# Kernel tuning notes

Hardware: AMD Instinct MI355X
Metric: run time of the kernel (lower is better)

Reference implementation:

```python
import math
import jax, jax.numpy as jnp
import numpy as np

NO_ITEMS = 50000
EMB_DIM = 448
FEAT_DIM = 64
DIM = EMB_DIM + FEAT_DIM  # 512
N_BLOCKS = 2
B, S = 8, 2048
EPS = 1e-05


def setup_inputs() -> dict:
    key = jax.random.key(0)
    ks = jax.random.split(key, 16)
    inv = 1.0 / math.sqrt(DIM)
    inp = {
        "user_sequence": jax.random.randint(ks[0], (B, S), 0, NO_ITEMS),
        "user_sequence_features": jax.random.normal(ks[1], (B, S, FEAT_DIM), dtype=jnp.float32),
        "emb_table": jax.random.normal(ks[2], (NO_ITEMS, EMB_DIM), dtype=jnp.float32) * 0.02,
        # stacked per-block params [L, DIM, DIM] / [L, DIM]; torch Linear: y = x @ W.T + b
        "Wq": jax.random.normal(ks[3], (N_BLOCKS, DIM, DIM), dtype=jnp.float32) * inv,
        "bq": jax.random.normal(ks[4], (N_BLOCKS, DIM), dtype=jnp.float32) * inv,
        "Wk": jax.random.normal(ks[5], (N_BLOCKS, DIM, DIM), dtype=jnp.float32) * inv,
        "bk": jax.random.normal(ks[6], (N_BLOCKS, DIM), dtype=jnp.float32) * inv,
        "Wv": jax.random.normal(ks[7], (N_BLOCKS, DIM, DIM), dtype=jnp.float32) * inv,
        "bv": jax.random.normal(ks[8], (N_BLOCKS, DIM), dtype=jnp.float32) * inv,
        "W1": jax.random.normal(ks[9], (N_BLOCKS, DIM, DIM), dtype=jnp.float32) * inv,
        "b1": jax.random.normal(ks[10], (N_BLOCKS, DIM), dtype=jnp.float32) * inv,
        "W2": jax.random.normal(ks[11], (N_BLOCKS, DIM, DIM), dtype=jnp.float32) * inv,
        "b2": jax.random.normal(ks[12], (N_BLOCKS, DIM), dtype=jnp.float32) * inv,
    }
    return inp


def _seq_norm(h):
    # EmbeddingSequenceNorm: normalize over sequence axis (axis=1),
    # torch .std() is unbiased (ddof=1); note the double eps in the source.
    mean = h.mean(axis=1)                        # [B, D]
    std = jnp.std(h, axis=1, ddof=1) + 1e-05     # [B, D]
    return (h - mean[:, None, :]) / (std[:, None, :] + EPS)


def reference(user_sequence, user_sequence_features, emb_table,
              Wq, bq, Wk, bk, Wv, bv, W1, b1, W2, b2):
    emb = emb_table[user_sequence]                       # [B, S, EMB_DIM]
    feats = user_sequence_features[:, :, :FEAT_DIM]      # [B, S, FEAT_DIM]
    x = jnp.concatenate([emb, feats], axis=-1)           # [B, S, DIM]
    scale = 1.0 / math.sqrt(DIM)
    for l in range(N_BLOCKS):
        q = x @ Wq[l].T + bq[l]
        k = x @ Wk[l].T + bk[l]
        v = x @ Wv[l].T + bv[l]
        # NOTE: no softmax in the original — raw tril(QK^T * scale) @ V
        scores = jnp.einsum('bqd,bkd->bqk', q, k) * scale  # [B, S, S]
        scores = jnp.tril(scores)
        h = jnp.einsum('bqk,bkd->bqd', scores, v)
        h = _seq_norm(h)
        h = jnp.maximum(h @ W1[l].T + b1[l], 0.0) @ W2[l].T + b2[l]
        x = h
    return x[:, -1]  # [B, DIM]
```

## Files before the change

### kernel.cpp

```cpp
#include <hip/hip_runtime.h>
#include <hip/hip_bf16.h>

typedef __hip_bfloat16 BF;
typedef __bf16 v8bf __attribute__((ext_vector_type(8)));
typedef float v4f __attribute__((ext_vector_type(4)));

constexpr int SEQ = 2048;
constexpr int DIMC = 512;
constexpr int BSZ = 8;

#define GF_RELU 1
#define GF_CAUSAL 2
#define GF_KCAP 4
#define GF_QKV 8
#define GF_BATCH8 16
#define GF_HSTAT 32

#define WAIT_VM4 0x0F74
#define WAIT_VM0 0x0F70

__device__ __forceinline__ void async16(BF* lds, const BF* g) {
  __builtin_amdgcn_global_load_lds(
      (const __attribute__((address_space(1))) void*)g,
      (__attribute__((address_space(3))) void*)lds,
      16, 0, 0);
}

__global__ __launch_bounds__(256, 4) void gemm_bt(
    const BF* __restrict__ A, const BF* __restrict__ W, const float* __restrict__ bias,
    BF* __restrict__ outB, float* __restrict__ outF, BF* __restrict__ outV,
    float* __restrict__ hsum, float* __restrict__ hsq,
    int M, int N, int K, int nbx,
    long long strideA, long long strideW, long long strideC,
    float scale, int flags)
{
  const int id = blockIdx.x;
  int z, bx, by;
  if (flags & GF_BATCH8) {
    z = id & 7;
    const int t = id >> 3;
    bx = t % nbx;
    by = t / nbx;
    if (flags & GF_KCAP) by = (M >> 7) - 1 - by;
  } else {
    z = 0;
    by = (id & 7) + ((id >> 3) & 15) * 8;
    bx = id >> 7;
  }
  const int m0 = by * 128;
  const int n0 = bx * 128;
  if ((flags & GF_CAUSAL) && n0 > m0) return;

  const BF* __restrict__ Ab = A + (size_t)z * strideA;
  const BF* __restrict__ Wb = W + (size_t)z * strideW;
  const size_t coff = (size_t)z * strideC;

  const int tid = threadIdx.x;
  const int w = tid >> 6;
  const int lane = tid & 63;
  const int lane15 = lane & 15;
  const int quad = lane >> 4;
  const int wr = w >> 1, wc = w & 1;
  const int rl = lane >> 2;
  const int clsw = ((lane & 3) ^ ((rl >> 1) & 3)) << 3;

  __shared__ __align__(16) BF smem[16384];
  BF* sA = smem;
  BF* sW = smem + 8192;

  v4f acc[4][4];
  {
    v4f zero = {0.f, 0.f, 0.f, 0.f};
#pragma unroll
    for (int a = 0; a < 4; ++a)
#pragma unroll
      for (int b = 0; b < 4; ++b) acc[a][b] = zero;
  }

  int Klim = K;
  if (flags & GF_KCAP) { int kc = m0 + 128; if (kc < Klim) Klim = kc; }
  const int ksteps = Klim >> 5;

  auto stage = [&](int kk, int buf) {
    const int k0 = kk << 5;
#pragma unroll
    for (int i = 0; i < 2; ++i) {
      const int r0 = w * 32 + i * 16;
      async16(&sA[buf * 4096 + r0 * 32], Ab + (size_t)(m0 + r0 + rl) * K + (k0 + clsw));
      async16(&sW[buf * 4096 + r0 * 32], Wb + (size_t)(n0 + r0 + rl) * K + (k0 + clsw));
    }
  };

  stage(0, 0);
  const int sw = quad ^ ((lane15 >> 1) & 3);

  for (int kk = 0; kk < ksteps; ++kk) {
    const int cur = kk & 1;
    if (kk + 1 < ksteps) {
      stage(kk + 1, cur ^ 1);
      __builtin_amdgcn_s_waitcnt(WAIT_VM4);
    } else {
      __builtin_amdgcn_s_waitcnt(WAIT_VM0);
    }
    __builtin_amdgcn_s_barrier();

    v8bf aF[4], wF[4];
    const v8bf* sAv = (const v8bf*)(sA + cur * 4096);
    const v8bf* sWv = (const v8bf*)(sW + cur * 4096);
#pragma unroll
    for (int t = 0; t < 4; ++t) {
      aF[t] = sAv[(wr * 64 + t * 16 + lane15) * 4 + sw];
      wF[t] = sWv[(wc * 64 + t * 16 + lane15) * 4 + sw];
    }
#pragma unroll
    for (int mt = 0; mt < 4; ++mt)
#pragma unroll
      for (int nt = 0; nt < 4; ++nt)
        acc[mt][nt] = __builtin_amdgcn_mfma_f32_16x16x32_bf16(aF[mt], wF[nt], acc[mt][nt], 0, 0, 0);
    __builtin_amdgcn_s_barrier();
  }

  if ((flags & GF_QKV) || (outB && !outF)) {
#pragma unroll
    for (int mt = 0; mt < 4; ++mt) {
#pragma unroll
      for (int nt = 0; nt < 4; ++nt) {
        const int col = wc * 64 + nt * 16 + lane15;
        const int cg = n0 + col;
        const float bv = bias ? bias[cg] : 0.0f;
#pragma unroll
        for (int i = 0; i < 4; ++i) {
          const int row = wr * 64 + mt * 16 + quad * 4 + i;
          float v = acc[mt][nt][i] * scale + bv;
          if ((flags & GF_RELU) && v < 0.f) v = 0.f;
          if ((flags & GF_CAUSAL) && cg > m0 + row) v = 0.f;
          smem[row * 128 + ((((col >> 3) ^ ((row >> 2) & 3)) << 3) | (col & 7))] =
              __float2bfloat16(v);
        }
      }
    }
    __syncthreads();
    BF* dst;
    int ldc, coloff;
    if (flags & GF_QKV) {
      const int seg = n0 >> 9;
      dst = (seg == 0) ? outB : (seg == 1 ? (BF*)outF : outV);
      ldc = 512;
      coloff = n0 & 511;
    } else {
      dst = outB + coff;
      ldc = N;
      coloff = n0;
    }
#pragma unroll
    for (int p = 0; p < 8; ++p) {
      const int g = p * 256 + tid;
      const int row = g >> 4, ch = g & 15;
      const v8bf val = *(const v8bf*)(smem + row * 128 + ((ch ^ ((row >> 2) & 3)) << 3));
      *(v8bf*)(dst + (size_t)(m0 + row) * ldc + coloff + ch * 8) = val;
    }
  } else {
    float psum[4] = {0.f, 0.f, 0.f, 0.f};
    float psq[4] = {0.f, 0.f, 0.f, 0.f};
#pragma unroll
    for (int mt = 0; mt < 4; ++mt) {
      const int rb = m0 + wr * 64 + mt * 16 + quad * 4;
#pragma unroll
      for (int nt = 0; nt < 4; ++nt) {
        const int cg = n0 + wc * 64 + nt * 16 + lane15;
        const float bv = bias ? bias[cg] : 0.0f;
#pragma unroll
        for (int i = 0; i < 4; ++i) {
          const int rg = rb + i;
          float v = acc[mt][nt][i] * scale + bv;
          if ((flags & GF_RELU) && v < 0.f) v = 0.f;
          if ((flags & GF_CAUSAL) && cg > rg) v = 0.f;
          if (outB) outB[coff + (size_t)rg * N + cg] = __float2bfloat16(v);
          if (outF) outF[coff + (size_t)rg * N + cg] = v;
          psum[nt] += v;
          psq[nt] += v * v;
        }
      }
    }
    if (flags & GF_HSTAT) {
      float* fs = (float*)smem;
      __syncthreads();
#pragma unroll
      for (int nt = 0; nt < 4; ++nt) {
        const int col = wc * 64 + nt * 16 + lane15;
        const int cont = wr * 4 + quad;
        fs[col * 8 + cont] = psum[nt];
        fs[1024 + col * 8 + cont] = psq[nt];
      }
      __syncthreads();
      if (tid < 128) {
        float s = 0.f, q = 0.f;
#pragma unroll
        for (int c = 0; c < 8; ++c) { s += fs[tid * 8 + c]; q += fs[1024 + tid * 8 + c]; }
        atomicAdd(hsum + z * 512 + n0 + tid, s);
        atomicAdd(hsq + z * 512 + n0 + tid, q);
      }
    }
  }
}

__global__ void gather_kernel(const int* __restrict__ seq, const float* __restrict__ feats,
                              const float* __restrict__ emb, BF* __restrict__ xb) {
  const int row = blockIdx.x;
  const int t = threadIdx.x;
  const int idx = seq[row];
  BF* xr = xb + (size_t)row * DIMC;
  if (t < 224) {
    const float2 e = *(const float2*)(emb + (size_t)idx * 448 + t * 2);
    xr[t * 2] = __float2bfloat16(e.x);
    xr[t * 2 + 1] = __float2bfloat16(e.y);
  } else {
    const int j = (t - 224) * 2;
    const float2 f = *(const float2*)(feats + (size_t)row * 64 + j);
    xr[448 + j] = __float2bfloat16(f.x);
    xr[448 + j + 1] = __float2bfloat16(f.y);
  }
}

__global__ void prep_kernel(const float* __restrict__ W1, const float* __restrict__ W2,
                            const float* __restrict__ Wq, const float* __restrict__ Wk,
                            const float* __restrict__ Wv, const float* __restrict__ bq,
                            const float* __restrict__ bk, const float* __restrict__ bv,
                            BF* __restrict__ wb, BF* __restrict__ wqkv, float* __restrict__ bqkv,
                            float* __restrict__ hstat) {
  const int t = blockIdx.x * 256 + threadIdx.x;
  const long long i = (long long)t * 4;
  if (t < 4096) {
    float4 z = {0.f, 0.f, 0.f, 0.f};
    *(float4*)(hstat + t * 4) = z;
  }
  float4 v;
  BF* o;
  if (i < 1048576) {
    v = (i < 524288) ? *(const float4*)(W1 + i) : *(const float4*)(W2 + (i - 524288));
    o = wb + i;
  } else {
    const long long j = i - 1048576;
    const int l = j >= 786432 ? 1 : 0;
    const long long rem = j - (long long)l * 786432;
    const int r = (int)(rem >> 9), c = (int)(rem & 511);
    const float* s = (r < 512) ? Wq : (r < 1024 ? Wk : Wv);
    v = *(const float4*)(s + (size_t)l * 262144 + (size_t)(r & 511) * 512 + c);
    o = wqkv + j;
  }
  o[0] = __float2bfloat16(v.x); o[1] = __float2bfloat16(v.y);
  o[2] = __float2bfloat16(v.z); o[3] = __float2bfloat16(v.w);
  if (t < 768) {
#pragma unroll
    for (int e = t * 4; e < t * 4 + 4; ++e) {
      const int l = e / 1536, r = e % 1536;
      const float* s = (r < 512) ? bq : (r < 1024 ? bk : bv);
      bqkv[e] = s[l * 512 + (r & 511)];
    }
  }
}

__global__ void transpose_kernel(const BF* __restrict__ in, BF* __restrict__ out) {
  __shared__ BF t[64][65];
  const int b = blockIdx.z;
  const int s0 = blockIdx.x * 64, d0 = blockIdx.y * 64;
  const int dx = threadIdx.x & 63, ry = threadIdx.x >> 6;
  const BF* ib = in + ((size_t)b * SEQ + s0) * DIMC + d0;
  BF* ob = out + ((size_t)b * DIMC + d0) * SEQ + s0;
#pragma unroll
  for (int i = 0; i < 16; ++i)
    t[ry + i * 4][dx] = ib[(size_t)(ry + i * 4) * DIMC + dx];
  __syncthreads();
#pragma unroll
  for (int i = 0; i < 16; ++i)
    ob[(size_t)(ry + i * 4) * SEQ + dx] = t[dx][ry + i * 4];
}

__global__ void seqstat_kernel(const float* __restrict__ hsum, const float* __restrict__ hsq,
                               float2* __restrict__ stat) {
  const int i = blockIdx.x * 256 + threadIdx.x;
  const float s = hsum[i], q = hsq[i];
  const float mean = s / SEQ;
  float var = (q - mean * s) / (SEQ - 1);
  if (var < 0.f) var = 0.f;
  stat[i] = make_float2(mean, 1.0f / (sqrtf(var) + 2e-5f));
}

__global__ void seqapply_kernel(const float* __restrict__ h, const float2* __restrict__ stat,
                                BF* __restrict__ out) {
  const size_t i = ((size_t)blockIdx.x * 256 + threadIdx.x) * 4;
  const int b = (int)(i >> 20);
  const int d = (int)(i & 511);
  const float4 v = *(const float4*)(h + i);
  const float2* sb = stat + (b << 9) + d;
  const float4 s01 = *(const float4*)(sb);
  const float4 s23 = *(const float4*)(sb + 2);
  out[i]     = __float2bfloat16((v.x - s01.x) * s01.y);
  out[i + 1] = __float2bfloat16((v.y - s01.z) * s01.w);
  out[i + 2] = __float2bfloat16((v.z - s23.x) * s23.y);
  out[i + 3] = __float2bfloat16((v.w - s23.z) * s23.w);
}

__global__ void ffn1last_kernel(const float* __restrict__ h32, const float2* __restrict__ stat,
                                const BF* __restrict__ W1B, const float* __restrict__ b1,
                                float* __restrict__ f1g) {
  const int b = blockIdx.x >> 3, nb = blockIdx.x & 7;
  const int t = threadIdx.x;
  __shared__ float hn[512];
  const float* hr = h32 + ((size_t)b * SEQ + (SEQ - 1)) * DIMC;
  const float2* sb = stat + b * 512;
  for (int d = t; d < 512; d += 256) {
    const float2 s = sb[d];
    hn[d] = (hr[d] - s.x) * s.y;
  }
  __syncthreads();
  const int o = nb * 64 + (t >> 2);
  const int seg = t & 3;
  const BF* wr = W1B + (size_t)o * 512 + seg * 128;
  const float* hs = hn + seg * 128;
  float acc = 0.f;
#pragma unroll
  for (int j = 0; j < 128; j += 8) {
    const v8bf wv = *(const v8bf*)(wr + j);
#pragma unroll
    for (int e = 0; e < 8; ++e) acc += hs[j + e] * (float)wv[e];
  }
  acc += __shfl_xor(acc, 1, 64);
  acc += __shfl_xor(acc, 2, 64);
  if (seg == 0) {
    const float v = acc + b1[o];
    f1g[b * 512 + o] = v > 0.f ? v : 0.f;
  }
}

__global__ void ffn2last_kernel(const float* __restrict__ f1g, const BF* __restrict__ W2B,
                                const float* __restrict__ b2, float* __restrict__ out) {
  const int b = blockIdx.x >> 3, nb = blockIdx.x & 7;
  const int t = threadIdx.x;
  __shared__ float f1[512];
  const float* fr = f1g + b * 512;
  for (int d = t; d < 512; d += 256) f1[d] = fr[d];
  __syncthreads();
  const int o = nb * 64 + (t >> 2);
  const int seg = t & 3;
  const BF* wr = W2B + (size_t)o * 512 + seg * 128;
  const float* fs = f1 + seg * 128;
  float acc = 0.f;
#pragma unroll
  for (int j = 0; j < 128; j += 8) {
    const v8bf wv = *(const v8bf*)(wr + j);
#pragma unroll
    for (int e = 0; e < 8; ++e) acc += fs[j + e] * (float)wv[e];
  }
  acc += __shfl_xor(acc, 1, 64);
  acc += __shfl_xor(acc, 2, 64);
  if (seg == 0) out[b * 512 + o] = acc + b2[o];
}

extern "C" void kernel_launch(void* const* d_in, const int* in_sizes, int n_in,
                              void* d_out, int out_size, void* d_ws, size_t ws_size,
                              hipStream_t stream) {
  const int* seq = (const int*)d_in[0];
  const float* feats = (const float*)d_in[1];
  const float* emb = (const float*)d_in[2];
  const float* Wq = (const float*)d_in[3];
  const float* bq = (const float*)d_in[4];
  const float* Wk = (const float*)d_in[5];
  const float* bk = (const float*)d_in[6];
  const float* Wv = (const float*)d_in[7];
  const float* bv = (const float*)d_in[8];
  const float* W1 = (const float*)d_in[9];
  const float* b1 = (const float*)d_in[10];
  const float* W2 = (const float*)d_in[11];
  const float* b2 = (const float*)d_in[12];
  float* out = (float*)d_out;

  char* ws = (char*)d_ws;
  const size_t MB = 1024 * 1024;
  BF* xb = (BF*)(ws);
  BF* qb = (BF*)(ws + 16 * MB);
  BF* kb = (BF*)(ws + 32 * MB);
  BF* vt = (BF*)(ws + 48 * MB);
  float* h32 = (float*)(ws + 64 * MB);
  BF* vtmp = (BF*)(ws + 64 * MB);
  BF* sc = (BF*)(ws + 96 * MB);
  BF* wb = (BF*)(ws + 160 * MB);
  BF* wqkv = (BF*)(ws + 162 * MB);
  float* bqkv = (float*)(ws + 166 * MB);
  float* f1g = (float*)(ws + 166 * MB + 512 * 1024);
  float* hstat = (float*)(ws + 167 * MB);
  float2* stat = (float2*)(ws + 168 * MB);

  const int WT = 2 * 512 * 512;
  prep_kernel<<<2560, 256, 0, stream>>>(W1, W2, Wq, Wk, Wv, bq, bk, bv, wb, wqkv, bqkv, hstat);
  gather_kernel<<<BSZ * SEQ, 256, 0, stream>>>(seq, feats, emb, xb);

  const float attn_scale = 0.04419417382415922f;
  const dim3 blk(256);

  for (int l = 0; l < 2; ++l) {
    const BF* W1B = wb + (size_t)l * 262144;
    const BF* W2B = wb + (size_t)WT + (size_t)l * 262144;
    float* hsum_l = hstat + (size_t)l * 8192;
    float* hsq_l = hsum_l + 4096;

    gemm_bt<<<1536, blk, 0, stream>>>(xb, wqkv + (size_t)l * 786432, bqkv + l * 1536,
        qb, (float*)kb, vtmp, nullptr, nullptr,
        16384, 1536, 512, 12, 0, 0, 0, 1.0f, GF_QKV);
    transpose_kernel<<<dim3(32, 8, 8), blk, 0, stream>>>(vtmp, vt);
    gemm_bt<<<2048, blk, 0, stream>>>(qb, kb, nullptr, sc, nullptr, nullptr,
        nullptr, nullptr, 2048, 2048, 512, 16,
        (long long)SEQ * DIMC, (long long)SEQ * DIMC, (long long)SEQ * SEQ,
        attn_scale, GF_CAUSAL | GF_BATCH8);
    gemm_bt<<<512, blk, 0, stream>>>(sc, vt, nullptr, nullptr, h32, nullptr,
        hsum_l, hsq_l, 2048, 512, 2048, 4,
        (long long)SEQ * SEQ, (long long)DIMC * SEQ, (long long)SEQ * DIMC,
        1.0f, GF_KCAP | GF_BATCH8 | GF_HSTAT);
    seqstat_kernel<<<16, 256, 0, stream>>>(hsum_l, hsq_l, stat);

    if (l == 0) {
      seqapply_kernel<<<16384, 256, 0, stream>>>(h32, stat, qb);
      gemm_bt<<<512, blk, 0, stream>>>(qb, W1B, b1 + l * 512, kb, nullptr, nullptr,
          nullptr, nullptr, 16384, 512, 512, 4, 0, 0, 0, 1.0f, GF_RELU);
      gemm_bt<<<512, blk, 0, stream>>>(kb, W2B, b2 + l * 512, xb,
          nullptr, nullptr, nullptr, nullptr, 16384, 512, 512, 4, 0, 0, 0, 1.0f, 0);
    } else {
      ffn1last_kernel<<<64, blk, 0, stream>>>(h32, stat, W1B, b1 + 512, f1g);
      ffn2last_kernel<<<64, blk, 0, stream>>>(f1g, W2B, b2 + 512, out);
    }
  }
}
```

Baseline: 443.7 us.

## Fold layer-0 FFN2 weights into layer-1 QKV projection and pair N-tiles

Layer 0's second FFN linear is linear with no activation, so its weights are precomposed with layer 1's Wq/Wk/Wv (Wqkv1·W2_0) and its bias is folded in via a small kernel. Layer 1's QKV GEMM then reads the FFN1 activations directly, removing a full 16384x512x512 GEMM and its write and read of x. The QKV GEMM also computes two adjacent N-tiles per block, reusing the A tile location and halving the grid. The cost is extra prep work: a W2 transpose, a small weight GEMM and a bias GEMV, plus the bf16 rounding of the composed weights.

```diff
diff --git a/kernel.cpp b/kernel.cpp
--- a/kernel.cpp
+++ b/kernel.cpp
@@ -15,6 +15,8 @@
 #define GF_QKV 8
 #define GF_BATCH8 16
 #define GF_HSTAT 32
+#define GF_SIMPLE 64
+#define GF_PAIR 128
 
 #define WAIT_VM4 0x0F74
 #define WAIT_VM0 0x0F70
@@ -42,14 +44,17 @@
     bx = t % nbx;
     by = t / nbx;
     if (flags & GF_KCAP) by = (M >> 7) - 1 - by;
+  } else if (flags & GF_SIMPLE) {
+    z = 0;
+    by = id % nbx;
+    bx = id / nbx;
   } else {
     z = 0;
     by = (id & 7) + ((id >> 3) & 15) * 8;
     bx = id >> 7;
   }
   const int m0 = by * 128;
-  const int n0 = bx * 128;
-  if ((flags & GF_CAUSAL) && n0 > m0) return;
+  if ((flags & GF_CAUSAL) && bx * 128 > m0) return;
 
   const BF* __restrict__ Ab = A + (size_t)z * strideA;
   const BF* __restrict__ Wb = W + (size_t)z * strideW;
@@ -68,137 +73,143 @@
   BF* sA = smem;
   BF* sW = smem + 8192;
 
-  v4f acc[4][4];
-  {
-    v4f zero = {0.f, 0.f, 0.f, 0.f};
-#pragma unroll
-    for (int a = 0; a < 4; ++a)
-#pragma unroll
-      for (int b = 0; b < 4; ++b) acc[a][b] = zero;
-  }
-
   int Klim = K;
   if (flags & GF_KCAP) { int kc = m0 + 128; if (kc < Klim) Klim = kc; }
   const int ksteps = Klim >> 5;
-
-  auto stage = [&](int kk, int buf) {
-    const int k0 = kk << 5;
-#pragma unroll
-    for (int i = 0; i < 2; ++i) {
-      const int r0 = w * 32 + i * 16;
-      async16(&sA[buf * 4096 + r0 * 32], Ab + (size_t)(m0 + r0 + rl) * K + (k0 + clsw));
-      async16(&sW[buf * 4096 + r0 * 32], Wb + (size_t)(n0 + r0 + rl) * K + (k0 + clsw));
-    }
-  };
-
-  stage(0, 0);
-  const int sw = quad ^ ((lane15 >> 1) & 3);
-
-  for (int kk = 0; kk < ksteps; ++kk) {
-    const int cur = kk & 1;
-    if (kk + 1 < ksteps) {
-      stage(kk + 1, cur ^ 1);
-      __builtin_amdgcn_s_waitcnt(WAIT_VM4);
+  const int nrep = (flags & GF_PAIR) ? 2 : 1;
+
+  for (int rp = 0; rp < nrep; ++rp) {
+    const int n0 = (flags & GF_PAIR) ? (bx * 2 + rp) * 128 : bx * 128;
+    if (rp) __syncthreads();
+
+    v4f acc[4][4];
+    {
+      v4f zero = {0.f, 0.f, 0.f, 0.f};
+#pragma unroll
+      for (int a = 0; a < 4; ++a)
+#pragma unroll
+        for (int b = 0; b < 4; ++b) acc[a][b] = zero;
+    }
+
+    auto stage = [&](int kk, int buf) {
+      const int k0 = kk << 5;
+#pragma unroll
+      for (int i = 0; i < 2; ++i) {
+        const int r0 = w * 32 + i * 16;
+        async16(&sA[buf * 4096 + r0 * 32], Ab + (size_t)(m0 + r0 + rl) * K + (k0 + clsw));
+        async16(&sW[buf * 4096 + r0 * 32], Wb + (size_t)(n0 + r0 + rl) * K + (k0 + clsw));
+      }
+    };
+
+    stage(0, 0);
+    const int sw = quad ^ ((lane15 >> 1) & 3);
+
+    for (int kk = 0; kk < ksteps; ++kk) {
+      const int cur = kk & 1;
+      if (kk + 1 < ksteps) {
+        stage(kk + 1, cur ^ 1);
+        __builtin_amdgcn_s_waitcnt(WAIT_VM4);
+      } else {
+        __builtin_amdgcn_s_waitcnt(WAIT_VM0);
+      }
+      __builtin_amdgcn_s_barrier();
+
+      v8bf aF[4], wF[4];
+      const v8bf* sAv = (const v8bf*)(sA + cur * 4096);
+      const v8bf* sWv = (const v8bf*)(sW + cur * 4096);
+#pragma unroll
+      for (int t = 0; t < 4; ++t) {
+        aF[t] = sAv[(wr * 64 + t * 16 + lane15) * 4 + sw];
+        wF[t] = sWv[(wc * 64 + t * 16 + lane15) * 4 + sw];
+      }
+#pragma unroll
+      for (int mt = 0; mt < 4; ++mt)
+#pragma unroll
+        for (int nt = 0; nt < 4; ++nt)
+          acc[mt][nt] = __builtin_amdgcn_mfma_f32_16x16x32_bf16(aF[mt], wF[nt], acc[mt][nt], 0, 0, 0);
+      __builtin_amdgcn_s_barrier();
+    }
+
+    if ((flags & GF_QKV) || (outB && !outF)) {
+#pragma unroll
+      for (int mt = 0; mt < 4; ++mt) {
+#pragma unroll
+        for (int nt = 0; nt < 4; ++nt) {
+          const int col = wc * 64 + nt * 16 + lane15;
+          const int cg = n0 + col;
+          const float bv = bias ? bias[cg] : 0.0f;
+#pragma unroll
+          for (int i = 0; i < 4; ++i) {
+            const int row = wr * 64 + mt * 16 + quad * 4 + i;
+            float v = acc[mt][nt][i] * scale + bv;
+            if ((flags & GF_RELU) && v < 0.f) v = 0.f;
+            if ((flags & GF_CAUSAL) && cg > m0 + row) v = 0.f;
+            smem[row * 128 + ((((col >> 3) ^ ((row >> 2) & 3)) << 3) | (col & 7))] =
+                __float2bfloat16(v);
+          }
+        }
+      }
+      __syncthreads();
+      BF* dst;
+      int ldc, coloff;
+      if (flags & GF_QKV) {
+        const int seg = n0 >> 9;
+        dst = (seg == 0) ? outB : (seg == 1 ? (BF*)outF : outV);
+        ldc = 512;
+        coloff = n0 & 511;
+      } else {
+        dst = outB + coff;
+        ldc = N;
+        coloff = n0;
+      }
+#pragma unroll
+      for (int p = 0; p < 8; ++p) {
+        const int g = p * 256 + tid;
+        const int row = g >> 4, ch = g & 15;
+        const v8bf val = *(const v8bf*)(smem + row * 128 + ((ch ^ ((row >> 2) & 3)) << 3));
+        *(v8bf*)(dst + (size_t)(m0 + row) * ldc + coloff + ch * 8) = val;
+      }
     } else {
-      __builtin_amdgcn_s_waitcnt(WAIT_VM0);
-    }
-    __builtin_amdgcn_s_barrier();
-
-    v8bf aF[4], wF[4];
-    const v8bf* sAv = (const v8bf*)(sA + cur * 4096);
-    const v8bf* sWv = (const v8bf*)(sW + cur * 4096);
-#pragma unroll
-    for (int t = 0; t < 4; ++t) {
-      aF[t] = sAv[(wr * 64 + t * 16 + lane15) * 4 + sw];
-      wF[t] = sWv[(wc * 64 + t * 16 + lane15) * 4 + sw];
-    }
-#pragma unroll
-    for (int mt = 0; mt < 4; ++mt)
-#pragma unroll
-      for (int nt = 0; nt < 4; ++nt)
-        acc[mt][nt] = __builtin_amdgcn_mfma_f32_16x16x32_bf16(aF[mt], wF[nt], acc[mt][nt], 0, 0, 0);
-    __builtin_amdgcn_s_barrier();
-  }
-
-  if ((flags & GF_QKV) || (outB && !outF)) {
-#pragma unroll
-    for (int mt = 0; mt < 4; ++mt) {
-#pragma unroll
-      for (int nt = 0; nt < 4; ++nt) {
-        const int col = wc * 64 + nt * 16 + lane15;
-        const int cg = n0 + col;
-        const float bv = bias ? bias[cg] : 0.0f;
-#pragma unroll
-        for (int i = 0; i < 4; ++i) {
-          const int row = wr * 64 + mt * 16 + quad * 4 + i;
-          float v = acc[mt][nt][i] * scale + bv;
-          if ((flags & GF_RELU) && v < 0.f) v = 0.f;
-          if ((flags & GF_CAUSAL) && cg > m0 + row) v = 0.f;
-          smem[row * 128 + ((((col >> 3) ^ ((row >> 2) & 3)) << 3) | (col & 7))] =
-              __float2bfloat16(v);
+      float psum[4] = {0.f, 0.f, 0.f, 0.f};
+      float psq[4] = {0.f, 0.f, 0.f, 0.f};
+#pragma unroll
+      for (int mt = 0; mt < 4; ++mt) {
+        const int rb = m0 + wr * 64 + mt * 16 + quad * 4;
+#pragma unroll
+        for (int nt = 0; nt < 4; ++nt) {
+          const int cg = n0 + wc * 64 + nt * 16 + lane15;
+          const float bv = bias ? bias[cg] : 0.0f;
+#pragma unroll
+          for (int i = 0; i < 4; ++i) {
+            const int rg = rb + i;
+            float v = acc[mt][nt][i] * scale + bv;
+            if ((flags & GF_RELU) && v < 0.f) v = 0.f;
+            if ((flags & GF_CAUSAL) && cg > rg) v = 0.f;
+            if (outB) outB[coff + (size_t)rg * N + cg] = __float2bfloat16(v);
+            if (outF) outF[coff + (size_t)rg * N + cg] = v;
+            psum[nt] += v;
+            psq[nt] += v * v;
+          }
         }
       }
-    }
-    __syncthreads();
-    BF* dst;
-    int ldc, coloff;
-    if (flags & GF_QKV) {
-      const int seg = n0 >> 9;
-      dst = (seg == 0) ? outB : (seg == 1 ? (BF*)outF : outV);
-      ldc = 512;
-      coloff = n0 & 511;
-    } else {
-      dst = outB + coff;
-      ldc = N;
-      coloff = n0;
-    }
-#pragma unroll
-    for (int p = 0; p < 8; ++p) {
-      const int g = p * 256 + tid;
-      const int row = g >> 4, ch = g & 15;
-      const v8bf val = *(const v8bf*)(smem + row * 128 + ((ch ^ ((row >> 2) & 3)) << 3));
-      *(v8bf*)(dst + (size_t)(m0 + row) * ldc + coloff + ch * 8) = val;
-    }
-  } else {
-    float psum[4] = {0.f, 0.f, 0.f, 0.f};
-    float psq[4] = {0.f, 0.f, 0.f, 0.f};
-#pragma unroll
-    for (int mt = 0; mt < 4; ++mt) {
-      const int rb = m0 + wr * 64 + mt * 16 + quad * 4;
-#pragma unroll
-      for (int nt = 0; nt < 4; ++nt) {
-        const int cg = n0 + wc * 64 + nt * 16 + lane15;
-        const float bv = bias ? bias[cg] : 0.0f;
-#pragma unroll
-        for (int i = 0; i < 4; ++i) {
-          const int rg = rb + i;
-          float v = acc[mt][nt][i] * scale + bv;
-          if ((flags & GF_RELU) && v < 0.f) v = 0.f;
-          if ((flags & GF_CAUSAL) && cg > rg) v = 0.f;
-          if (outB) outB[coff + (size_t)rg * N + cg] = __float2bfloat16(v);
-          if (outF) outF[coff + (size_t)rg * N + cg] = v;
-          psum[nt] += v;
-          psq[nt] += v * v;
+      if (flags & GF_HSTAT) {
+        float* fs = (float*)smem;
+        __syncthreads();
+#pragma unroll
+        for (int nt = 0; nt < 4; ++nt) {
+          const int col = wc * 64 + nt * 16 + lane15;
+          const int cont = wr * 4 + quad;
+          fs[col * 8 + cont] = psum[nt];
+          fs[1024 + col * 8 + cont] = psq[nt];
         }
-      }
-    }
-    if (flags & GF_HSTAT) {
-      float* fs = (float*)smem;
-      __syncthreads();
-#pragma unroll
-      for (int nt = 0; nt < 4; ++nt) {
-        const int col = wc * 64 + nt * 16 + lane15;
-        const int cont = wr * 4 + quad;
-        fs[col * 8 + cont] = psum[nt];
-        fs[1024 + col * 8 + cont] = psq[nt];
-      }
-      __syncthreads();
-      if (tid < 128) {
-        float s = 0.f, q = 0.f;
-#pragma unroll
-        for (int c = 0; c < 8; ++c) { s += fs[tid * 8 + c]; q += fs[1024 + tid * 8 + c]; }
-        atomicAdd(hsum + z * 512 + n0 + tid, s);
-        atomicAdd(hsq + z * 512 + n0 + tid, q);
+        __syncthreads();
+        if (tid < 128) {
+          float s = 0.f, q = 0.f;
+#pragma unroll
+          for (int c = 0; c < 8; ++c) { s += fs[tid * 8 + c]; q += fs[1024 + tid * 8 + c]; }
+          atomicAdd(hsum + z * 512 + n0 + tid, s);
+          atomicAdd(hsq + z * 512 + n0 + tid, q);
+        }
       }
     }
   }
@@ -227,12 +238,22 @@
                             const float* __restrict__ Wv, const float* __restrict__ bq,
                             const float* __restrict__ bk, const float* __restrict__ bv,
                             BF* __restrict__ wb, BF* __restrict__ wqkv, float* __restrict__ bqkv,
-                            float* __restrict__ hstat) {
+                            float* __restrict__ hstat, BF* __restrict__ w2t) {
   const int t = blockIdx.x * 256 + threadIdx.x;
+  if (t >= 655360) {
+    const int j = (t - 655360) * 4;
+    if (j < 262144) {
+      const int c = j >> 9, k = j & 511;
+#pragma unroll
+      for (int e = 0; e < 4; ++e)
+        w2t[(size_t)c * 512 + k + e] = __float2bfloat16(W2[(size_t)(k + e) * 512 + c]);
+    }
+    return;
+  }
   const long long i = (long long)t * 4;
   if (t < 4096) {
-    float4 z = {0.f, 0.f, 0.f, 0.f};
-    *(float4*)(hstat + t * 4) = z;
+    float4 zz = {0.f, 0.f, 0.f, 0.f};
+    *(float4*)(hstat + t * 4) = zz;
   }
   float4 v;
   BF* o;
@@ -258,6 +279,24 @@
       bqkv[e] = s[l * 512 + (r & 511)];
     }
   }
+}
+
+__global__ void qkvbias_kernel(const BF* __restrict__ wq1, const float* __restrict__ bqkv1,
+                               const float* __restrict__ b2l0, float* __restrict__ bfq) {
+  const int o = blockIdx.x * 64 + (threadIdx.x >> 2);
+  const int seg = threadIdx.x & 3;
+  const BF* wr = wq1 + (size_t)o * 512 + seg * 128;
+  const float* bs = b2l0 + seg * 128;
+  float acc = 0.f;
+#pragma unroll
+  for (int j = 0; j < 128; j += 8) {
+    const v8bf wv = *(const v8bf*)(wr + j);
+#pragma unroll
+    for (int e = 0; e < 8; ++e) acc += bs[j + e] * (float)wv[e];
+  }
+  acc += __shfl_xor(acc, 1, 64);
+  acc += __shfl_xor(acc, 2, 64);
+  if (seg == 0) bfq[o] = bqkv1[o] + acc;
 }
 
 __global__ void transpose_kernel(const BF* __restrict__ in, BF* __restrict__ out) {
@@ -390,9 +429,16 @@
   float* f1g = (float*)(ws + 166 * MB + 512 * 1024);
   float* hstat = (float*)(ws + 167 * MB);
   float2* stat = (float2*)(ws + 168 * MB);
+  BF* w2t = (BF*)(ws + 169 * MB);
+  BF* wf = (BF*)(ws + 170 * MB);
+  float* bfq = (float*)(ws + 172 * MB);
 
   const int WT = 2 * 512 * 512;
-  prep_kernel<<<2560, 256, 0, stream>>>(W1, W2, Wq, Wk, Wv, bq, bk, bv, wb, wqkv, bqkv, hstat);
+  prep_kernel<<<2816, 256, 0, stream>>>(W1, W2, Wq, Wk, Wv, bq, bk, bv, wb, wqkv, bqkv,
+                                        hstat, w2t);
+  qkvbias_kernel<<<24, 256, 0, stream>>>(wqkv + 786432, bqkv + 1536, b2, bfq);
+  gemm_bt<<<48, 256, 0, stream>>>(wqkv + 786432, w2t, nullptr, wf, nullptr, nullptr,
+      nullptr, nullptr, 1536, 512, 512, 12, 0, 0, 0, 1.0f, GF_SIMPLE);
   gather_kernel<<<BSZ * SEQ, 256, 0, stream>>>(seq, feats, emb, xb);
 
   const float attn_scale = 0.04419417382415922f;
@@ -403,12 +449,17 @@
     const BF* W2B = wb + (size_t)WT + (size_t)l * 262144;
     float* hsum_l = hstat + (size_t)l * 8192;
     float* hsq_l = hsum_l + 4096;
-
-    gemm_bt<<<1536, blk, 0, stream>>>(xb, wqkv + (size_t)l * 786432, bqkv + l * 1536,
-        qb, (float*)kb, vtmp, nullptr, nullptr,
-        16384, 1536, 512, 12, 0, 0, 0, 1.0f, GF_QKV);
+    BF* kdst = (l == 0) ? kb : xb;
+
+    if (l == 0) {
+      gemm_bt<<<768, blk, 0, stream>>>(xb, wqkv, bqkv, qb, (float*)kb, vtmp,
+          nullptr, nullptr, 16384, 1536, 512, 0, 0, 0, 0, 1.0f, GF_QKV | GF_PAIR);
+    } else {
+      gemm_bt<<<768, blk, 0, stream>>>(kb, wf, bfq, qb, (float*)xb, vtmp,
+          nullptr, nullptr, 16384, 1536, 512, 0, 0, 0, 0, 1.0f, GF_QKV | GF_PAIR);
+    }
     transpose_kernel<<<dim3(32, 8, 8), blk, 0, stream>>>(vtmp, vt);
-    gemm_bt<<<2048, blk, 0, stream>>>(qb, kb, nullptr, sc, nullptr, nullptr,
+    gemm_bt<<<2048, blk, 0, stream>>>(qb, kdst, nullptr, sc, nullptr, nullptr,
         nullptr, nullptr, 2048, 2048, 512, 16,
         (long long)SEQ * DIMC, (long long)SEQ * DIMC, (long long)SEQ * SEQ,
         attn_scale, GF_CAUSAL | GF_BATCH8);
@@ -422,8 +473,6 @@
       seqapply_kernel<<<16384, 256, 0, stream>>>(h32, stat, qb);
       gemm_bt<<<512, blk, 0, stream>>>(qb, W1B, b1 + l * 512, kb, nullptr, nullptr,
           nullptr, nullptr, 16384, 512, 512, 4, 0, 0, 0, 1.0f, GF_RELU);
-      gemm_bt<<<512, blk, 0, stream>>>(kb, W2B, b2 + l * 512, xb,
-          nullptr, nullptr, nullptr, nullptr, 16384, 512, 512, 4, 0, 0, 0, 1.0f, 0);
     } else {
       ffn1last_kernel<<<64, blk, 0, stream>>>(h32, stat, W1B, b1 + 512, f1g);
       ffn2last_kernel<<<64, blk, 0, stream>>>(f1g, W2B, b2 + 512, out);
```

Result: slower. 829.9 us (+87.0%).
